# Performance work log

Hardware: AMD Instinct MI355X
Metric: run time of the kernel (lower is better)

Reference implementation:

```python
import jax, jax.numpy as jnp
import numpy as np

B, F, T, Z, Y, X = 1, 8, 5, 16, 96, 96
N_RAYS = 32768   # n_rays_scan
K = 128          # n_points_ray
NEAR_PLANE = 0.01
C = F * Z        # conv channels after folding Z into channel dim


def setup_inputs() -> dict:
    key = jax.random.key(0)
    ks = jax.random.split(key, 6)
    vol = jax.random.normal(ks[0], (B, F, T, Z, Y, X), jnp.float32)
    # ray origins inside the normalized unit-cube scene
    rays_o = jax.random.uniform(ks[1], (T, N_RAYS, 3), jnp.float32, 0.1, 0.9)
    rd = jax.random.normal(ks[2], (T, N_RAYS, 3), jnp.float32)
    rays_d = rd / jnp.linalg.norm(rd, axis=-1, keepdims=True)
    conv_w = jax.random.normal(ks[3], (C, C, 3, 3, 3), jnp.float32) * (1.0 / np.sqrt(C * 27))
    conv_b = jnp.zeros((C,), jnp.float32)
    dens_w = jax.random.normal(ks[4], (F, 1), jnp.float32) * (1.0 / np.sqrt(F))
    dens_b = jnp.zeros((1,), jnp.float32)
    return dict(curr_feat_volume=vol, ray_start=rays_o, ray_direction=rays_d,
                conv_w=conv_w, conv_b=conv_b, dens_w=dens_w, dens_b=dens_b)


def _trilinear(vol, pts):
    """vol: [F,Z,Y,X]; pts: [...,3] with (x,y,z) in [0,1]. Returns [..., F]."""
    Fc, Zs, Ys, Xs = vol.shape
    gx = jnp.clip(pts[..., 0], 0.0, 1.0) * (Xs - 1)
    gy = jnp.clip(pts[..., 1], 0.0, 1.0) * (Ys - 1)
    gz = jnp.clip(pts[..., 2], 0.0, 1.0) * (Zs - 1)
    x0 = jnp.floor(gx).astype(jnp.int32); x1 = jnp.minimum(x0 + 1, Xs - 1)
    y0 = jnp.floor(gy).astype(jnp.int32); y1 = jnp.minimum(y0 + 1, Ys - 1)
    z0 = jnp.floor(gz).astype(jnp.int32); z1 = jnp.minimum(z0 + 1, Zs - 1)
    fx = gx - x0; fy = gy - y0; fz = gz - z0
    out = 0.0
    for zi, wz in ((z0, 1 - fz), (z1, fz)):
        for yi, wy in ((y0, 1 - fy), (y1, fy)):
            for xi, wx in ((x0, 1 - fx), (x1, fx)):
                out = out + vol[:, zi, yi, xi] * (wz * wy * wx)[None]
    return jnp.moveaxis(out, 0, -1)


def _render_t(vol_t, o, d, dens_w, dens_b):
    """One timestep: vol_t [F,Z,Y,X], o/d [N,3] -> depth [N,1]."""
    # SceneCollider: AABB [0,1]^3 with near_plane clamp
    t1 = (0.0 - o) / d
    t2 = (1.0 - o) / d
    near = jnp.max(jnp.minimum(t1, t2), axis=-1, keepdims=True)
    far = jnp.min(jnp.maximum(t1, t2), axis=-1, keepdims=True)
    near = jnp.maximum(near, NEAR_PLANE)
    far = jnp.maximum(far, near + 1e-6)
    # UniformSampler (deterministic bins)
    bins = jnp.linspace(0.0, 1.0, K + 1, dtype=jnp.float32)
    ts = near + bins[None, :] * (far - near)          # [N,K+1]
    starts = ts[:, :-1, None]                          # [N,K,1]
    ends = ts[:, 1:, None]
    mids = 0.5 * (starts + ends)
    pts = o[:, None, :] + d[:, None, :] * mids         # [N,K,3]
    # DensityField: trilinear feature gather + linear + softplus
    feats = _trilinear(vol_t, pts)                     # [N,K,F]
    density = jax.nn.softplus(feats @ dens_w + dens_b) # [N,K,1]
    # weights / transmittance (alpha compositing)
    deltas = ends - starts
    dd = density * deltas
    trans = jnp.exp(-jnp.concatenate([jnp.zeros_like(dd[:, :1]),
                                      jnp.cumsum(dd[:, :-1], axis=1)], axis=1))
    alpha = 1.0 - jnp.exp(-dd)
    weights = alpha * trans                            # [N,K,1]
    # DepthRenderer
    eps = 1e-10
    depth = jnp.sum(weights * starts, axis=-2) / (jnp.sum(weights, axis=-2) + eps)
    depth = jnp.clip(depth, starts.min(), starts.max())
    return depth                                       # [N,1]


def reference(curr_feat_volume, ray_start, ray_direction, conv_w, conv_b, dens_w, dens_b):
    # fold Z into channels and run dense Conv3d over (T,Y,X)
    x = jnp.transpose(curr_feat_volume, (0, 1, 3, 2, 4, 5)).reshape(B, F * Z, T, Y, X)
    y = jax.lax.conv_general_dilated(
        x, conv_w, window_strides=(1, 1, 1), padding='SAME',
        dimension_numbers=('NCDHW', 'OIDHW', 'NCDHW'))
    y = y + conv_b[None, :, None, None, None]
    future = jnp.transpose(y.reshape(B, F, Z, T, Y, X), (0, 3, 1, 2, 4, 5))  # [B,T,F,Z,Y,X]
    vols = future[0]                                   # [T,F,Z,Y,X]
    depth = jax.vmap(lambda v, o, d: _render_t(v, o, d, dens_w, dens_b))(
        vols, ray_start, ray_direction)                # [T,N,1]
    return depth
```

## Files before the change

kernel.cpp:

```cpp
#include <hip/hip_runtime.h>
#include <hip/hip_fp16.h>
#include <cstdint>
#include <cstddef>

#define T_DIM 5
#define F_DIM 8
#define Z_DIM 16
#define Y_DIM 96
#define X_DIM 96
#define NRAYS 32768
#define K_SAMP 128


struct __align__(16) Cell { __half2 h0, h1, h2, h3; };

typedef __attribute__((ext_vector_type(4))) float     f32x4;
typedef __attribute__((ext_vector_type(8))) _Float16  f16x8;

__global__ __launch_bounds__(256) void prep_w_kernel(
        const float* __restrict__ w, const float* __restrict__ cb,
        const float* __restrict__ dw,
        __half* __restrict__ wB, float* __restrict__ bR,
        unsigned* loU, unsigned* hiU) {
    int i = blockIdx.x * 256 + threadIdx.x;
    if (i < 8) { loU[i] = 0x7F800000u; hiU[i] = 0u; }
    if (i < 16) {
        float s = 0.f;
        #pragma unroll
        for (int f = 0; f < 8; ++f) s += cb[f * 16 + i] * dw[f];
        bR[i] = s;
    }
    int cs  = i & 31;
    int zo  = (i >> 5) & 15;
    int pt  = i >> 9;
    int p   = pt / 27;
    int tap = pt - p * 27;
    int ci  = p * 32 + cs;
    float s = 0.f;
    #pragma unroll
    for (int f = 0; f < 8; ++f)
        s += w[(size_t)((f * 16 + zo) * 128 + ci) * 27 + tap] * dw[f];
    wB[i] = __float2half(s);
}

__global__ __launch_bounds__(256) void transpose_vol_kernel(
        const float* __restrict__ xin, __half* __restrict__ inp) {
    __shared__ __half lds[96 * 136];
    int b = blockIdx.x;
    int t = b / 96, y = b - (b / 96) * 96;
    for (int i = threadIdx.x; i < 12288; i += 256) {
        int row = i / 96;
        int x   = i - row * 96;
        int f = row >> 4, z = row & 15;
        float v = xin[(((size_t)(f * 5 + t) * 16 + z) * 96 + y) * 96 + x];
        lds[x * 136 + row] = __float2half(v);
    }
    __syncthreads();
    __half* ob = inp + ((size_t)(t * 96 + y) * 96) * 128;
    for (int c = threadIdx.x; c < 1536; c += 256) {
        int x = c >> 4, sub = c & 15;
        uint4 v = *(const uint4*)(lds + x * 136 + sub * 8);
        *(uint4*)(ob + (size_t)x * 128 + sub * 8) = v;
    }
}

__global__ __launch_bounds__(256) void nearfar_kernel(
        const float* __restrict__ ro, const float* __restrict__ rd,
        float* __restrict__ nearA, float* __restrict__ farA,
        unsigned* loU, unsigned* hiU) {
    int gid = blockIdx.x * 256 + threadIdx.x;
    int t = gid / NRAYS;
    const float* o = ro + (size_t)gid * 3;
    const float* d = rd + (size_t)gid * 3;
    float ox = o[0], oy = o[1], oz = o[2];
    float dx = d[0], dy = d[1], dz = d[2];
    float t1x = (0.f - ox) / dx, t2x = (1.f - ox) / dx;
    float t1y = (0.f - oy) / dy, t2y = (1.f - oy) / dy;
    float t1z = (0.f - oz) / dz, t2z = (1.f - oz) / dz;
    float nr = fmaxf(fmaxf(fminf(t1x, t2x), fminf(t1y, t2y)), fminf(t1z, t2z));
    float fr = fminf(fminf(fmaxf(t1x, t2x), fmaxf(t1y, t2y)), fmaxf(t1z, t2z));
    nr = fmaxf(nr, 0.01f);
    fr = fmaxf(fr, nr + 1e-6f);
    nearA[gid] = nr;
    farA[gid]  = fr;
    float slast = fmaf(0.9921875f, fr - nr, nr);
    float mn = nr, mx = slast;
    #pragma unroll
    for (int off = 32; off > 0; off >>= 1) {
        mn = fminf(mn, __shfl_down(mn, off, 64));
        mx = fmaxf(mx, __shfl_down(mx, off, 64));
    }
    __shared__ float smn[4], smx[4];
    int w = threadIdx.x >> 6;
    if ((threadIdx.x & 63) == 0) { smn[w] = mn; smx[w] = mx; }
    __syncthreads();
    if (threadIdx.x == 0) {
        mn = fminf(fminf(smn[0], smn[1]), fminf(smn[2], smn[3]));
        mx = fmaxf(fmaxf(smx[0], smx[1]), fmaxf(smx[2], smx[3]));
        atomicMin(&loU[t], __float_as_uint(mn));
        atomicMax(&hiU[t], __float_as_uint(mx));
    }
}

__global__ __launch_bounds__(128) void conv_mfma_kernel(
        const __half* __restrict__ inp, const __half* __restrict__ wB,
        const float* __restrict__ bR, float* __restrict__ fld) {
    int bid = blockIdx.x;
    int wg  = (bid & 7) * 90 + (bid >> 3);
    int xs  = wg % 3;
    int rem = wg / 3;
    int yp  = rem % 48;
    int t   = rem / 48;
    int xseg = xs * 32, y0 = yp * 2;

    __shared__ __half lds[12 * 34 * 32];
    const int w    = threadIdx.x >> 6;
    const int lane = threadIdx.x & 63;
    const int l15  = lane & 15;
    const int ksub = lane >> 4;

    f32x4 acc0 = {0.f, 0.f, 0.f, 0.f};
    f32x4 acc1 = {0.f, 0.f, 0.f, 0.f};

    for (int p = 0; p < 4; ++p) {
        for (int c = threadIdx.x; c < 1632; c += 128) {
            int row = c / 136;
            int r2  = c - row * 136;
            int xl  = r2 >> 2, sub = r2 & 3;
            int tt = t  + (row >> 2) - 1;
            int yy = y0 + (row & 3)  - 1;
            int xg = xseg + xl - 1;
            uint4 v = {0u, 0u, 0u, 0u};
            if ((unsigned)tt < 5u && (unsigned)yy < 96u && (unsigned)xg < 96u)
                v = *(const uint4*)(inp + ((((size_t)tt * 96 + yy) * 96 + xg) << 7)
                                        + (p << 5) + (sub << 3));
            *(uint4*)(lds + (size_t)c * 8) = v;
        }
        __syncthreads();

        const __half* wp_base = wB + (size_t)p * 13824 + l15 * 32 + ksub * 8;
        #pragma unroll
        for (int kt = 0; kt < 3; ++kt) {
            #pragma unroll
            for (int ky = 0; ky < 3; ++ky) {
                const __half* lrow = lds + (kt * 4 + w + ky) * 1088 + ksub * 8;
                #pragma unroll
                for (int kx = 0; kx < 3; ++kx) {
                    int tap = (kt * 3 + ky) * 3 + kx;
                    f16x8 aw = *(const f16x8*)(wp_base + tap * 512);
                    f16x8 b0 = *(const f16x8*)(lrow + (l15 + kx) * 32);
                    acc0 = __builtin_amdgcn_mfma_f32_16x16x32_f16(aw, b0, acc0, 0, 0, 0);
                    f16x8 b1 = *(const f16x8*)(lrow + (l15 + kx + 16) * 32);
                    acc1 = __builtin_amdgcn_mfma_f32_16x16x32_f16(aw, b1, acc1, 0, 0, 0);
                }
            }
        }
        __syncthreads();
    }

    int yw = y0 + w;
    #pragma unroll
    for (int r = 0; r < 4; ++r) {
        int zo = ksub * 4 + r;
        float bz = bR[zo];
        size_t o = (((size_t)t * 16 + zo) * 96 + yw) * 96 + xseg + l15;
        fld[o]      = acc0[r] + bz;
        fld[o + 16] = acc1[r] + bz;
    }
}

__global__ __launch_bounds__(256) void pack_kernel(
        const float* __restrict__ fld, Cell* __restrict__ cellp) {
    int i = blockIdx.x * 256 + threadIdx.x;
    if (i >= 737280) return;
    int x = i % 96;
    int r = i / 96;
    int y = r % 96;
    int r2 = r / 96;
    int z = r2 % 16;
    int t = r2 / 16;
    const float* ft = fld + (size_t)t * 147456;
    int xp = min(x + 1, 95);
    int yr0 = y * 96, yr1 = min(y + 1, 95) * 96;
    int zr0 = z * 9216, zr1 = min(z + 1, 15) * 9216;
    float c000 = ft[zr0 + yr0 + x], c001 = ft[zr0 + yr0 + xp];
    float c010 = ft[zr0 + yr1 + x], c011 = ft[zr0 + yr1 + xp];
    float c100 = ft[zr1 + yr0 + x], c101 = ft[zr1 + yr0 + xp];
    float c110 = ft[zr1 + yr1 + x], c111 = ft[zr1 + yr1 + xp];
    Cell cl;
    cl.h0 = __floats2half2_rn(c000, c001);
    cl.h1 = __floats2half2_rn(c010, c011);
    cl.h2 = __floats2half2_rn(c100, c101);
    cl.h3 = __floats2half2_rn(c110, c111);
    cellp[i] = cl;
}

__global__ __launch_bounds__(256) void render_kernel(
        const float* __restrict__ ro, const float* __restrict__ rd,
        const Cell* __restrict__ cellp,
        const float* __restrict__ nearA, const float* __restrict__ farA,
        const unsigned* __restrict__ loU, const unsigned* __restrict__ hiU,
        const float* __restrict__ dens_b, float* __restrict__ out) {
    int b = blockIdx.x;
    int b7 = b & 7, bhi = b >> 3;
    int t, seg;
    if (b7 < 5) { t = b7; seg = bhi; }
    else { int j = (b7 - 5) * 320 + bhi; t = j / 192; seg = 320 + j % 192; }
    int c = threadIdx.x & 3;
    int ray = t * NRAYS + seg * 64 + (threadIdx.x >> 2);

    const float* o = ro + (size_t)ray * 3;
    const float* d = rd + (size_t)ray * 3;
    float ox = o[0], oy = o[1], oz = o[2];
    float dx = d[0], dy = d[1], dz = d[2];
    float nr = nearA[ray], fr = farA[ray];
    float span = fr - nr;
    const Cell* vt = cellp + (size_t)t * 147456;
    float db = dens_b[0];

    float step = span * 0.0078125f;
    float s  = fmaf((float)(c * 32), step, nr);
    float mid = s + 0.5f * step;
    float px = fmaf(dx, mid, ox);
    float py = fmaf(dy, mid, oy);
    float pz = fmaf(dz, mid, oz);
    float ddx = dx * step, ddy = dy * step, ddz = dz * step;

    float num = 0.f, den = 0.f, A = 0.f;
    float trans = 1.f;
    int pidx = -1;
    float2 f00 = {0.f, 0.f}, f01 = {0.f, 0.f}, f10 = {0.f, 0.f}, f11 = {0.f, 0.f};
    for (int kk = 0; kk < 32; ++kk) {
        float gx = fminf(fmaxf(px, 0.f), 1.f) * 95.f;
        float gy = fminf(fmaxf(py, 0.f), 1.f) * 95.f;
        float gz = fminf(fmaxf(pz, 0.f), 1.f) * 15.f;
        int x0 = min((int)gx, 94), y0 = min((int)gy, 94), z0 = min((int)gz, 14);
        float fx = gx - (float)x0, fy = gy - (float)y0, fz = gz - (float)z0;

        int idx = z0 * 9216 + y0 * 96 + x0;
        if (idx != pidx) {
            pidx = idx;
            Cell cl = vt[idx];
            f00 = __half22float2(cl.h0);
            f01 = __half22float2(cl.h1);
            f10 = __half22float2(cl.h2);
            f11 = __half22float2(cl.h3);
        }

        float v00 = f00.x + fx * (f00.y - f00.x);
        float v01 = f01.x + fx * (f01.y - f01.x);
        float v10 = f10.x + fx * (f10.y - f10.x);
        float v11 = f11.x + fx * (f11.y - f11.x);
        float v0  = v00 + fy * (v01 - v00);
        float v1  = v10 + fy * (v11 - v10);
        float pre = v0 + fz * (v1 - v0) + db;

        float u = __expf(-fabsf(pre));
        float dens = fmaxf(pre, 0.f) + __logf(1.f + u);
        float dd = dens * step;
        float ex = __expf(-dd);
        float wgt = (1.f - ex) * trans;
        num = fmaf(wgt, s, num);
        den += wgt;
        trans *= ex;
        A += dd;
        s += step; px += ddx; py += ddy; pz += ddz;
    }
    int lane = threadIdx.x & 63;
    int q = lane & ~3;
    float A0 = __shfl(A, q,     64);
    float A1 = __shfl(A, q + 1, 64);
    float A2 = __shfl(A, q + 2, 64);
    float P = 0.f;
    if (c > 0) P += A0;
    if (c > 1) P += A1;
    if (c > 2) P += A2;
    float sc = __expf(-P);
    float numc = num * sc;
    float denc = den * sc;
    numc += __shfl_xor(numc, 1, 64);
    numc += __shfl_xor(numc, 2, 64);
    denc += __shfl_xor(denc, 1, 64);
    denc += __shfl_xor(denc, 2, 64);
    if (c == 0) {
        float depth = numc / (denc + 1e-10f);
        float lo = __uint_as_float(loU[t]);
        float hi = __uint_as_float(hiU[t]);
        depth = fminf(fmaxf(depth, lo), hi);
        out[ray] = depth;
    }
}

extern "C" void kernel_launch(void* const* d_in, const int* in_sizes, int n_in,
                              void* d_out, int out_size, void* d_ws, size_t ws_size,
                              hipStream_t stream) {
    const float* vol = (const float*)d_in[0];
    const float* ro  = (const float*)d_in[1];
    const float* rd  = (const float*)d_in[2];
    const float* cw  = (const float*)d_in[3];
    const float* cb  = (const float*)d_in[4];
    const float* dw  = (const float*)d_in[5];
    const float* dbp = (const float*)d_in[6];
    float* out = (float*)d_out;

    float* ws      = (float*)d_ws;
    float* fld     = ws;
    __half* inp    = (__half*)(ws + 737280);
    Cell*  cellp   = (Cell*)(ws + 737280);
    __half* wB     = (__half*)(ws + 737280 + 2949120);
    float* bR      = ws + 737280 + 2949120 + 27648;
    float* nearA   = bR + 32;
    float* farA    = nearA + 163840;
    unsigned* loU  = (unsigned*)(farA + 163840);
    unsigned* hiU  = loU + 8;

    hipLaunchKernelGGL(prep_w_kernel, dim3(216), dim3(256), 0, stream,
                       cw, cb, dw, wB, bR, loU, hiU);
    hipLaunchKernelGGL(transpose_vol_kernel, dim3(480), dim3(256), 0, stream, vol, inp);
    hipLaunchKernelGGL(nearfar_kernel, dim3(640), dim3(256), 0, stream,
                       ro, rd, nearA, farA, loU, hiU);
    hipLaunchKernelGGL(conv_mfma_kernel, dim3(720), dim3(128), 0, stream,
                       inp, wB, bR, fld);
    hipLaunchKernelGGL(pack_kernel, dim3(2880), dim3(256), 0, stream, fld, cellp);
    hipLaunchKernelGGL(render_kernel, dim3(2560), dim3(256), 0, stream,
                       ro, rd, cellp, nearA, farA, loU, hiU, dbp, out);
}
```

Before: 195.4 us.

## Swizzle conv LDS tile, precompute cell deltas, use base-2 exp/log in render

The conv kernel's LDS fill loop is rewritten as a fixed 12-row unrolled copy with precomputed per-thread offsets. It applies an XOR swizzle on the 8-half sub-blocks so the MFMA B-operand reads avoid LDS bank conflicts. The cell-packing kernel now stores the x-difference instead of the second corner, so the render loop saves one subtract per corner pair. The render loop drops its cached-cell branch, folds the grid scale into the position increments, and works in base 2 via native exp2/log2 intrinsics. This trims ALU and divergence but reloads the cell every sample, and storing fp16 differences slightly changes rounding.

```diff
diff --git a/kernel.cpp b/kernel.cpp
--- a/kernel.cpp
+++ b/kernel.cpp
@@ -16,6 +16,9 @@
 
 typedef __attribute__((ext_vector_type(4))) float     f32x4;
 typedef __attribute__((ext_vector_type(8))) _Float16  f16x8;
+
+__device__ __forceinline__ float fexp2(float x) { return __builtin_amdgcn_exp2f(x); }
+__device__ __forceinline__ float flog2(float x) { return __builtin_amdgcn_logf(x); }
 
 __global__ __launch_bounds__(256) void prep_w_kernel(
         const float* __restrict__ w, const float* __restrict__ cb,
@@ -119,22 +122,50 @@
     const int l15  = lane & 15;
     const int ksub = lane >> 4;
 
+    const int xl0 = threadIdx.x >> 2, sub0 = threadIdx.x & 3;
+    const int xg0 = xseg + xl0 - 1;
+    const bool xok0 = (unsigned)xg0 < 96u;
+    const int glo0 = xg0 * 128 + sub0 * 8;
+    const int lof0 = xl0 * 32 + ((sub0 ^ ((xl0 >> 1) & 3)) << 3);
+    const int hl   = threadIdx.x;
+    const int xl1 = 32 + (hl >> 2), sub1 = hl & 3;
+    const int xg1 = xseg + xl1 - 1;
+    const bool xok1 = (unsigned)xg1 < 96u;
+    const int glo1 = xg1 * 128 + sub1 * 8;
+    const int lof1 = xl1 * 32 + ((sub1 ^ ((xl1 >> 1) & 3)) << 3);
+
+    int offA[3];
+    #pragma unroll
+    for (int kx = 0; kx < 3; ++kx) {
+        int X = l15 + kx;
+        offA[kx] = X * 32 + ((ksub ^ ((X >> 1) & 3)) << 3);
+    }
+
     f32x4 acc0 = {0.f, 0.f, 0.f, 0.f};
     f32x4 acc1 = {0.f, 0.f, 0.f, 0.f};
 
     for (int p = 0; p < 4; ++p) {
-        for (int c = threadIdx.x; c < 1632; c += 128) {
-            int row = c / 136;
-            int r2  = c - row * 136;
-            int xl  = r2 >> 2, sub = r2 & 3;
-            int tt = t  + (row >> 2) - 1;
-            int yy = y0 + (row & 3)  - 1;
-            int xg = xseg + xl - 1;
+        #pragma unroll
+        for (int r = 0; r < 12; ++r) {
+            int tt = t + (r >> 2) - 1;
+            int yy = y0 + (r & 3) - 1;
+            bool rok = ((unsigned)tt < 5u) & ((unsigned)yy < 96u);
+            int rbase = (tt * 96 + yy) * 12288 + (p << 5);
             uint4 v = {0u, 0u, 0u, 0u};
-            if ((unsigned)tt < 5u && (unsigned)yy < 96u && (unsigned)xg < 96u)
-                v = *(const uint4*)(inp + ((((size_t)tt * 96 + yy) * 96 + xg) << 7)
-                                        + (p << 5) + (sub << 3));
-            *(uint4*)(lds + (size_t)c * 8) = v;
+            if (rok & xok0) v = *(const uint4*)(inp + rbase + glo0);
+            *(uint4*)(lds + r * 1088 + lof0) = v;
+        }
+        if (threadIdx.x < 8) {
+            #pragma unroll
+            for (int r = 0; r < 12; ++r) {
+                int tt = t + (r >> 2) - 1;
+                int yy = y0 + (r & 3) - 1;
+                bool rok = ((unsigned)tt < 5u) & ((unsigned)yy < 96u);
+                int rbase = (tt * 96 + yy) * 12288 + (p << 5);
+                uint4 v = {0u, 0u, 0u, 0u};
+                if (rok & xok1) v = *(const uint4*)(inp + rbase + glo1);
+                *(uint4*)(lds + r * 1088 + lof1) = v;
+            }
         }
         __syncthreads();
 
@@ -143,14 +174,14 @@
         for (int kt = 0; kt < 3; ++kt) {
             #pragma unroll
             for (int ky = 0; ky < 3; ++ky) {
-                const __half* lrow = lds + (kt * 4 + w + ky) * 1088 + ksub * 8;
+                const __half* lrow = lds + (kt * 4 + w + ky) * 1088;
                 #pragma unroll
                 for (int kx = 0; kx < 3; ++kx) {
                     int tap = (kt * 3 + ky) * 3 + kx;
                     f16x8 aw = *(const f16x8*)(wp_base + tap * 512);
-                    f16x8 b0 = *(const f16x8*)(lrow + (l15 + kx) * 32);
+                    f16x8 b0 = *(const f16x8*)(lrow + offA[kx]);
                     acc0 = __builtin_amdgcn_mfma_f32_16x16x32_f16(aw, b0, acc0, 0, 0, 0);
-                    f16x8 b1 = *(const f16x8*)(lrow + (l15 + kx + 16) * 32);
+                    f16x8 b1 = *(const f16x8*)(lrow + offA[kx] + 512);
                     acc1 = __builtin_amdgcn_mfma_f32_16x16x32_f16(aw, b1, acc1, 0, 0, 0);
                 }
             }
@@ -188,10 +219,10 @@
     float c100 = ft[zr1 + yr0 + x], c101 = ft[zr1 + yr0 + xp];
     float c110 = ft[zr1 + yr1 + x], c111 = ft[zr1 + yr1 + xp];
     Cell cl;
-    cl.h0 = __floats2half2_rn(c000, c001);
-    cl.h1 = __floats2half2_rn(c010, c011);
-    cl.h2 = __floats2half2_rn(c100, c101);
-    cl.h3 = __floats2half2_rn(c110, c111);
+    cl.h0 = __floats2half2_rn(c000, c001 - c000);
+    cl.h1 = __floats2half2_rn(c010, c011 - c010);
+    cl.h2 = __floats2half2_rn(c100, c101 - c100);
+    cl.h3 = __floats2half2_rn(c110, c111 - c110);
     cellp[i] = cl;
 }
 
@@ -214,68 +245,57 @@
     float ox = o[0], oy = o[1], oz = o[2];
     float dx = d[0], dy = d[1], dz = d[2];
     float nr = nearA[ray], fr = farA[ray];
-    float span = fr - nr;
     const Cell* vt = cellp + (size_t)t * 147456;
-    float db = dens_b[0];
-
-    float step = span * 0.0078125f;
+    const float L2E = 1.4426950408889634f;
+    float db2 = dens_b[0] * L2E;
+
+    float step = (fr - nr) * 0.0078125f;
     float s  = fmaf((float)(c * 32), step, nr);
     float mid = s + 0.5f * step;
-    float px = fmaf(dx, mid, ox);
-    float py = fmaf(dy, mid, oy);
-    float pz = fmaf(dz, mid, oz);
-    float ddx = dx * step, ddy = dy * step, ddz = dz * step;
-
-    float num = 0.f, den = 0.f, A = 0.f;
+    float pxg = fmaf(dx, mid, ox) * 95.f;
+    float pyg = fmaf(dy, mid, oy) * 95.f;
+    float pzg = fmaf(dz, mid, oz) * 15.f;
+    float ddxg = dx * step * 95.f, ddyg = dy * step * 95.f, ddzg = dz * step * 15.f;
+
+    float num = 0.f, den = 0.f, A2 = 0.f;
     float trans = 1.f;
-    int pidx = -1;
-    float2 f00 = {0.f, 0.f}, f01 = {0.f, 0.f}, f10 = {0.f, 0.f}, f11 = {0.f, 0.f};
     for (int kk = 0; kk < 32; ++kk) {
-        float gx = fminf(fmaxf(px, 0.f), 1.f) * 95.f;
-        float gy = fminf(fmaxf(py, 0.f), 1.f) * 95.f;
-        float gz = fminf(fmaxf(pz, 0.f), 1.f) * 15.f;
+        float gx = fminf(fmaxf(pxg, 0.f), 95.f);
+        float gy = fminf(fmaxf(pyg, 0.f), 95.f);
+        float gz = fminf(fmaxf(pzg, 0.f), 15.f);
         int x0 = min((int)gx, 94), y0 = min((int)gy, 94), z0 = min((int)gz, 14);
         float fx = gx - (float)x0, fy = gy - (float)y0, fz = gz - (float)z0;
 
-        int idx = z0 * 9216 + y0 * 96 + x0;
-        if (idx != pidx) {
-            pidx = idx;
-            Cell cl = vt[idx];
-            f00 = __half22float2(cl.h0);
-            f01 = __half22float2(cl.h1);
-            f10 = __half22float2(cl.h2);
-            f11 = __half22float2(cl.h3);
-        }
-
-        float v00 = f00.x + fx * (f00.y - f00.x);
-        float v01 = f01.x + fx * (f01.y - f01.x);
-        float v10 = f10.x + fx * (f10.y - f10.x);
-        float v11 = f11.x + fx * (f11.y - f11.x);
-        float v0  = v00 + fy * (v01 - v00);
-        float v1  = v10 + fy * (v11 - v10);
-        float pre = v0 + fz * (v1 - v0) + db;
-
-        float u = __expf(-fabsf(pre));
-        float dens = fmaxf(pre, 0.f) + __logf(1.f + u);
-        float dd = dens * step;
-        float ex = __expf(-dd);
+        Cell cl = vt[z0 * 9216 + y0 * 96 + x0];
+        float v00 = fmaf(fx, __half2float(__high2half(cl.h0)), __half2float(__low2half(cl.h0)));
+        float v01 = fmaf(fx, __half2float(__high2half(cl.h1)), __half2float(__low2half(cl.h1)));
+        float v10 = fmaf(fx, __half2float(__high2half(cl.h2)), __half2float(__low2half(cl.h2)));
+        float v11 = fmaf(fx, __half2float(__high2half(cl.h3)), __half2float(__low2half(cl.h3)));
+        float v0  = fmaf(fy, v01 - v00, v00);
+        float v1  = fmaf(fy, v11 - v10, v10);
+        float pre2 = fmaf(fmaf(fz, v1 - v0, v0), L2E, db2);
+
+        float u = fexp2(-fabsf(pre2));
+        float dens2 = fmaxf(pre2, 0.f) + flog2(1.f + u);
+        float dd2 = dens2 * step;
+        float ex = fexp2(-dd2);
         float wgt = (1.f - ex) * trans;
         num = fmaf(wgt, s, num);
         den += wgt;
         trans *= ex;
-        A += dd;
-        s += step; px += ddx; py += ddy; pz += ddz;
+        A2 += dd2;
+        s += step; pxg += ddxg; pyg += ddyg; pzg += ddzg;
     }
     int lane = threadIdx.x & 63;
     int q = lane & ~3;
-    float A0 = __shfl(A, q,     64);
-    float A1 = __shfl(A, q + 1, 64);
-    float A2 = __shfl(A, q + 2, 64);
+    float A0 = __shfl(A2, q,     64);
+    float A1 = __shfl(A2, q + 1, 64);
+    float Ab = __shfl(A2, q + 2, 64);
     float P = 0.f;
     if (c > 0) P += A0;
     if (c > 1) P += A1;
-    if (c > 2) P += A2;
-    float sc = __expf(-P);
+    if (c > 2) P += Ab;
+    float sc = fexp2(-P);
     float numc = num * sc;
     float denc = den * sc;
     numc += __shfl_xor(numc, 1, 64);
```

Result: slower. 212.4 us (+8.7%).
